# Kernel optimization log

Hardware: AMD Instinct MI355X
Metric: run time of the kernel (lower is better)

## Reference

```python
import jax, jax.numpy as jnp
import numpy as np

M = 256       # number of chart centers
D = 512       # feature dim
B = 131072    # batch of encoder features
R = 32.0      # chart radius (~sqrt(2*D) for whitened random data)
TAU = 0.01    # center EMA rate
EPS = 1e-6


def setup_inputs() -> dict:
    key = jax.random.key(0)
    k0, k1, k2, k3 = jax.random.split(key, 4)
    z = jax.random.normal(k0, (B, D), dtype=jnp.float32)
    centers = jax.random.normal(k1, (M, D), dtype=jnp.float32)
    stats_mean = 0.1 * jax.random.normal(k2, (D,), dtype=jnp.float32)
    stats_var = jax.random.uniform(k3, (D,), dtype=jnp.float32, minval=0.5, maxval=1.5)
    return {"z": z, "centers": centers, "stats_mean": stats_mean, "stats_var": stats_var}


def _whiten(z, mean, var):
    return (z - mean) / jnp.sqrt(var + EPS)


def _cdist(z_w, centers):
    # ||a-c||^2 = ||a||^2 + ||c||^2 - 2 a.c   (avoids [B,M,D] intermediate)
    zn = jnp.sum(z_w * z_w, axis=1)            # [B]
    cn = jnp.sum(centers * centers, axis=1)     # [M]
    d2 = zn[:, None] + cn[None, :] - 2.0 * (z_w @ centers.T)  # [B, M]
    return jnp.sqrt(jnp.maximum(d2, 0.0))


def reference(z, centers, stats_mean, stats_var):
    # memberships(): whiten + cdist + argmin + radius masks
    z_w = _whiten(z, stats_mean, stats_var)     # [B, D]
    dists = _cdist(z_w, centers)                # [B, M]
    hard_idx = jnp.argmin(dists, axis=1)        # [B]
    masks = dists <= R                          # [B, M] bool (masks[:, i] == torch masks[i])

    # soft_update_centers(): scatter-mean of z_w per nearest cluster, EMA update
    counts = jax.ops.segment_sum(jnp.ones((z_w.shape[0],), z_w.dtype), hard_idx, num_segments=M)  # [M]
    sums = jax.ops.segment_sum(z_w, hard_idx, num_segments=M)                                     # [M, D]
    mean_i = sums / jnp.maximum(counts, 1.0)[:, None]
    has_members = (counts > 0)[:, None]
    new_centers = jnp.where(has_members, (1.0 - TAU) * centers + TAU * mean_i, centers)

    return dists, hard_idx, masks, new_centers
```

## Files before the change

kernel.cpp:

```cpp
#include <hip/hip_runtime.h>
#include <math.h>

#define M_CENTERS 256
#define D_DIM     512
#define B_BATCH   131072
#define RADIUS    32.0f
#define TAU_F     0.01f
#define EPS_F     1e-6f

#define DMARGIN 2.0e-2f
#define REF_BLOCKS 1024
#define UCHUNKS 16
#define NCHUNK 16
#define SC_ROWS 1024

typedef __attribute__((ext_vector_type(8))) short bf16x8;
typedef __attribute__((ext_vector_type(16))) float f32x16;

__device__ __forceinline__ unsigned short bf16h(float x) {
    unsigned int u = __float_as_uint(x);
    return (unsigned short)((u + 0x7fffu + ((u >> 16) & 1u)) >> 16);
}
__device__ __forceinline__ unsigned cvt_pk_bf16(float a, float b) {
    unsigned r;
    asm("v_cvt_pk_bf16_f32 %0, %1, %2" : "=v"(r) : "v"(a), "v"(b));
    return r;
}

__global__ void prep_ss_kernel(const float* __restrict__ mean, const float* __restrict__ var,
                               float* __restrict__ scale, float* __restrict__ shift) {
    int d = blockIdx.x * 256 + threadIdx.x;
    if (d < D_DIM) {
        float s = 1.0f / sqrtf(var[d] + EPS_F);
        scale[d] = s;
        shift[d] = -mean[d] * s;
    }
}

__global__ void prep_cb_kernel(const float* __restrict__ centers, unsigned char* __restrict__ img,
                               float* __restrict__ cn) {
    int c = blockIdx.x;
    int l = threadIdx.x;
    int kc = l >> 2, kq = l & 3;
    const float* cp = centers + (size_t)c * D_DIM + kc * 32 + kq * 8;
    float4 a = *reinterpret_cast<const float4*>(cp);
    float4 b = *reinterpret_cast<const float4*>(cp + 4);
    float s = a.x*a.x + a.y*a.y + a.z*a.z + a.w*a.w + b.x*b.x + b.y*b.y + b.z*b.z + b.w*b.w;
    #pragma unroll
    for (int off = 32; off >= 1; off >>= 1) s += __shfl_xor(s, off, 64);
    if (l == 0) cn[c] = s;

    unsigned h0 = cvt_pk_bf16(a.x, a.y);
    unsigned h1 = cvt_pk_bf16(a.z, a.w);
    unsigned h2 = cvt_pk_bf16(b.x, b.y);
    unsigned h3 = cvt_pk_bf16(b.z, b.w);
    *reinterpret_cast<uint4*>(img + (size_t)kc * 16384 + (size_t)kq * 4096 + (size_t)c * 16) =
        make_uint4(h0, h1, h2, h3);
}

__global__ __launch_bounds__(256, 4)
void dist_mfma_kernel(const float* __restrict__ z,
                      const unsigned char* __restrict__ cb_img,
                      const float* __restrict__ scale, const float* __restrict__ shift,
                      const float* __restrict__ cn,
                      float* __restrict__ out_dists, float* __restrict__ out_idxf,
                      float* __restrict__ out_masks, int* __restrict__ ws_idx,
                      int* __restrict__ counts,
                      int* __restrict__ amb_count, int* __restrict__ amb_rows) {
    __shared__ union {
        struct { unsigned char A[2][4096]; unsigned char B[2][16384]; } p;
        float bounce[2][16][256];
        struct { float znrow[64]; float rminS[64][2]; int ridxS[64][2];
                 int rcntS[64][2]; float fminS[64]; int lhist[M_CENTERS]; } e;
    } sm;

    const int tid = threadIdx.x;
    const int wv = tid >> 6, lane = tid & 63;
    const int rt = wv >> 1, ch = wv & 1;
    const int l31 = lane & 31, kg = lane >> 5;
    const int b0 = blockIdx.x * 64;

    const int arow = tid >> 2, akq = tid & 3;
    const float* zrow = z + (size_t)(b0 + arow) * D_DIM;

    f32x16 acc[4];
    #pragma unroll
    for (int n = 0; n < 4; ++n)
        #pragma unroll
        for (int r = 0; r < 16; ++r) acc[n][r] = 0.0f;
    float zsq = 0.0f;
    float4 zv, zv2, scv, scv2, shv, shv2;

    auto stage_load = [&](int kc, int cb) {
        const unsigned char* bsrc = cb_img + (size_t)kc * 16384 + (size_t)wv * 4096;
        unsigned char* bdst = &sm.p.B[cb][wv * 4096];
        #pragma unroll
        for (int r = 0; r < 4; ++r) {
            __builtin_amdgcn_global_load_lds(
                (const __attribute__((address_space(1))) unsigned int*)(bsrc + r * 1024 + (lane << 4)),
                (__attribute__((address_space(3))) unsigned int*)(bdst + r * 1024),
                16, 0, 0);
        }
        const int kf = kc * 32 + akq * 8;
        zv   = *reinterpret_cast<const float4*>(zrow + kf);
        zv2  = *reinterpret_cast<const float4*>(zrow + kf + 4);
        scv  = *reinterpret_cast<const float4*>(scale + kf);
        scv2 = *reinterpret_cast<const float4*>(scale + kf + 4);
        shv  = *reinterpret_cast<const float4*>(shift + kf);
        shv2 = *reinterpret_cast<const float4*>(shift + kf + 4);
    };
    auto stage_write = [&](int cb) {
        float w0 = fmaf(zv.x,  scv.x,  shv.x);
        float w1 = fmaf(zv.y,  scv.y,  shv.y);
        float w2 = fmaf(zv.z,  scv.z,  shv.z);
        float w3 = fmaf(zv.w,  scv.w,  shv.w);
        float w4 = fmaf(zv2.x, scv2.x, shv2.x);
        float w5 = fmaf(zv2.y, scv2.y, shv2.y);
        float w6 = fmaf(zv2.z, scv2.z, shv2.z);
        float w7 = fmaf(zv2.w, scv2.w, shv2.w);
        zsq = fmaf(w0, w0, fmaf(w1, w1, fmaf(w2, w2, fmaf(w3, w3, zsq))));
        zsq = fmaf(w4, w4, fmaf(w5, w5, fmaf(w6, w6, fmaf(w7, w7, zsq))));
        uint4 hv = make_uint4(cvt_pk_bf16(w0, w1), cvt_pk_bf16(w2, w3),
                              cvt_pk_bf16(w4, w5), cvt_pk_bf16(w6, w7));
        *reinterpret_cast<uint4*>(&sm.p.A[cb][akq * 1024 + arow * 16]) = hv;
    };

    stage_load(0, 0);
    stage_write(0);
    __syncthreads();

    int cc = 0;
    for (int kc = 0; kc < NCHUNK; ++kc) {
        const bool pf = (kc + 1 < NCHUNK);
        if (pf) stage_load(kc + 1, cc ^ 1);
        const unsigned char* Ab = &sm.p.A[cc][0];
        const unsigned char* Bb = &sm.p.B[cc][0];
        const int arow16 = (rt * 32 + l31) * 16;
        bf16x8 a0 = *reinterpret_cast<const bf16x8*>(Ab + (0 * 2 + kg) * 1024 + arow16);
        bf16x8 a1 = *reinterpret_cast<const bf16x8*>(Ab + (1 * 2 + kg) * 1024 + arow16);
        #pragma unroll
        for (int n = 0; n < 4; ++n) {
            const int bcol16 = (ch * 128 + n * 32 + l31) * 16;
            bf16x8 b0 = *reinterpret_cast<const bf16x8*>(Bb + (0 * 2 + kg) * 4096 + bcol16);
            bf16x8 b1 = *reinterpret_cast<const bf16x8*>(Bb + (1 * 2 + kg) * 4096 + bcol16);
            acc[n] = __builtin_amdgcn_mfma_f32_32x32x16_bf16(a0, b0, acc[n], 0, 0, 0);
            acc[n] = __builtin_amdgcn_mfma_f32_32x32x16_bf16(a1, b1, acc[n], 0, 0, 0);
        }
        if (pf) stage_write(cc ^ 1);
        __syncthreads();
        cc ^= 1;
    }

    zsq += __shfl_xor(zsq, 1, 64);
    zsq += __shfl_xor(zsq, 2, 64);
    if (akq == 0) sm.e.znrow[arow] = zsq;
    sm.e.lhist[tid] = 0;
    __syncthreads();

    float znv[16];
    #pragma unroll
    for (int r = 0; r < 16; ++r) znv[r] = sm.e.znrow[rt * 32 + 4 * kg + (r & 3) + 8 * (r >> 2)];
    float cnv[4];
    #pragma unroll
    for (int n = 0; n < 4; ++n) cnv[n] = cn[ch * 128 + n * 32 + l31];

    #pragma unroll
    for (int n = 0; n < 4; ++n)
        #pragma unroll
        for (int r = 0; r < 16; ++r) {
            float d2 = znv[r] + cnv[n] - 2.0f * acc[n][r];
            acc[n][r] = sqrtf(fmaxf(d2, 0.0f));
        }

    #pragma unroll
    for (int r = 0; r < 16; ++r) {
        float bd = 3.4e38f; int bi = 0;
        #pragma unroll
        for (int n = 0; n < 4; ++n) {
            float d = acc[n][r];
            int col = ch * 128 + n * 32 + l31;
            if (d < bd) { bd = d; bi = col; }
        }
        #pragma unroll
        for (int off = 1; off <= 16; off <<= 1) {
            float od = __shfl_xor(bd, off, 64);
            int   oi = __shfl_xor(bi, off, 64);
            if (od < bd || (od == bd && oi < bi)) { bd = od; bi = oi; }
        }
        if (l31 == 0) {
            int R = rt * 32 + 4 * kg + (r & 3) + 8 * (r >> 2);
            sm.e.rminS[R][ch] = bd; sm.e.ridxS[R][ch] = bi;
        }
    }
    __syncthreads();
    if (tid < 64) {
        float d0 = sm.e.rminS[tid][0], d1 = sm.e.rminS[tid][1];
        int i0 = sm.e.ridxS[tid][0], i1 = sm.e.ridxS[tid][1];
        float fd = d0; int fi = i0;
        if (d1 < d0 || (d1 == d0 && i1 < i0)) { fd = d1; fi = i1; }
        sm.e.fminS[tid] = fd;
        out_idxf[b0 + tid] = (float)fi;
        ws_idx[b0 + tid] = fi;
        atomicAdd(&sm.e.lhist[fi], 1);
    }
    __syncthreads();
    #pragma unroll
    for (int r = 0; r < 16; ++r) {
        int R = rt * 32 + 4 * kg + (r & 3) + 8 * (r >> 2);
        float thr = sm.e.fminS[R] + DMARGIN;
        int cnt = 0;
        #pragma unroll
        for (int n = 0; n < 4; ++n) cnt += (acc[n][r] <= thr) ? 1 : 0;
        #pragma unroll
        for (int off = 1; off <= 16; off <<= 1) cnt += __shfl_xor(cnt, off, 64);
        if (l31 == 0) sm.e.rcntS[R][ch] = cnt;
    }
    __syncthreads();
    if (tid < 64) {
        if (sm.e.rcntS[tid][0] + sm.e.rcntS[tid][1] > 1) {
            int p = atomicAdd(amb_count, 1);
            if (p < B_BATCH) amb_rows[p] = b0 + tid;
        }
    }
    if (sm.e.lhist[tid] > 0) atomicAdd(&counts[tid], sm.e.lhist[tid]);

    #pragma unroll
    for (int hp = 0; hp < 2; ++hp) {
        __syncthreads();
        #pragma unroll
        for (int rr = 0; rr < 8; ++rr) {
            const int r = hp * 8 + rr;
            const int Rl = 4 * kg + (r & 3) + 8 * (r >> 2) - hp * 16;
            #pragma unroll
            for (int n = 0; n < 4; ++n)
                sm.bounce[rt][Rl][ch * 128 + n * 32 + l31] = acc[n][r];
        }
        __syncthreads();
        #pragma unroll
        for (int i = 0; i < 8; ++i) {
            const int Rl = ch * 8 + i;
            float4 dq = *reinterpret_cast<const float4*>(&sm.bounce[rt][Rl][lane * 4]);
            const int grow = b0 + rt * 32 + hp * 16 + Rl;
            size_t ob = (size_t)grow * M_CENTERS + lane * 4;
            *reinterpret_cast<float4*>(out_dists + ob) = dq;
            float4 mq = make_float4(dq.x <= RADIUS ? 1.0f : 0.0f, dq.y <= RADIUS ? 1.0f : 0.0f,
                                    dq.z <= RADIUS ? 1.0f : 0.0f, dq.w <= RADIUS ? 1.0f : 0.0f);
            *reinterpret_cast<float4*>(out_masks + ob) = mq;
        }
    }
}

__global__ __launch_bounds__(64)
void refine_kernel(const float* __restrict__ z, const float* __restrict__ centers,
                   const float* __restrict__ smean, const float* __restrict__ svar,
                   const float* __restrict__ dists,
                   const int* __restrict__ amb_count, const int* __restrict__ amb_rows,
                   float* __restrict__ out_idxf, int* __restrict__ ws_idx,
                   int* __restrict__ counts) {
    const int lane = threadIdx.x;
    int n = *amb_count;
    if (n > B_BATCH) n = B_BATCH;
    for (int e = blockIdx.x; e < n; e += REF_BLOCKS) {
        const int row = amb_rows[e];
        float4 dq = *reinterpret_cast<const float4*>(dists + (size_t)row * M_CENTERS + lane * 4);
        float dl[4] = { dq.x, dq.y, dq.z, dq.w };
        float dmin = fminf(fminf(dl[0], dl[1]), fminf(dl[2], dl[3]));
        #pragma unroll
        for (int off = 32; off >= 1; off >>= 1) dmin = fminf(dmin, __shfl_xor(dmin, off, 64));

        float zwf[8];
        double zn = 0.0;
        {
            float4 za = *reinterpret_cast<const float4*>(z + (size_t)row * D_DIM + lane * 8);
            float4 zb = *reinterpret_cast<const float4*>(z + (size_t)row * D_DIM + lane * 8 + 4);
            float zr[8] = { za.x, za.y, za.z, za.w, zb.x, zb.y, zb.z, zb.w };
            #pragma unroll
            for (int k = 0; k < 8; ++k) {
                int d = lane * 8 + k;
                float w = (zr[k] - smean[d]) / sqrtf(svar[d] + EPS_F);
                zwf[k] = w;
                zn += (double)w * (double)w;
            }
        }
        #pragma unroll
        for (int off = 32; off >= 1; off >>= 1) zn += __shfl_xor(zn, off, 64);
        const float zn32 = (float)zn;

        float bestd = 3.4e38f;
        int bestj = M_CENTERS;
        #pragma unroll
        for (int q = 0; q < 4; ++q) {
            unsigned long long mask = __ballot(dl[q] <= dmin + DMARGIN);
            while (mask) {
                int b = __ffsll(mask) - 1;
                mask &= mask - 1;
                int j = b * 4 + q;
                float4 ca = *reinterpret_cast<const float4*>(centers + (size_t)j * D_DIM + lane * 8);
                float4 cb = *reinterpret_cast<const float4*>(centers + (size_t)j * D_DIM + lane * 8 + 4);
                float cr[8] = { ca.x, ca.y, ca.z, ca.w, cb.x, cb.y, cb.z, cb.w };
                double dot = 0.0, cnl = 0.0;
                #pragma unroll
                for (int k = 0; k < 8; ++k) {
                    double c = (double)cr[k];
                    dot += (double)zwf[k] * c;
                    cnl += c * c;
                }
                #pragma unroll
                for (int off = 32; off >= 1; off >>= 1) {
                    dot += __shfl_xor(dot, off, 64);
                    cnl += __shfl_xor(cnl, off, 64);
                }
                float cn32  = (float)cnl;
                float dot32 = (float)dot;
                float t1  = zn32 + cn32;
                float d2f = t1 - 2.0f * dot32;
                d2f = fmaxf(d2f, 0.0f);
                float df = sqrtf(d2f);
                if (df < bestd || (df == bestd && j < bestj)) { bestd = df; bestj = j; }
            }
        }
        if (lane == 0) {
            int old = ws_idx[row];
            if (old != bestj) {
                atomicSub(&counts[old], 1);
                atomicAdd(&counts[bestj], 1);
                out_idxf[row] = (float)bestj;
                ws_idx[row]   = bestj;
            }
        }
    }
}

__global__ void scan_kernel(const int* __restrict__ counts, int* __restrict__ offsets,
                            int* __restrict__ cursor) {
    __shared__ int s[M_CENTERS];
    int t = threadIdx.x;
    int c = counts[t];
    s[t] = c;
    __syncthreads();
    for (int off = 1; off < M_CENTERS; off <<= 1) {
        int v = (t >= off) ? s[t - off] : 0;
        __syncthreads();
        s[t] += v;
        __syncthreads();
    }
    int excl = s[t] - c;
    offsets[t] = excl;
    cursor[t]  = excl;
    if (t == M_CENTERS - 1) offsets[M_CENTERS] = s[t];
}

__global__ __launch_bounds__(256)
void scatter2_kernel(const int* __restrict__ idx, int* __restrict__ cursor,
                     int* __restrict__ order) {
    __shared__ int lh[M_CENTERS];
    __shared__ int lb[M_CENTERS];
    const int t = threadIdx.x;
    lh[t] = 0;
    __syncthreads();
    const int base = blockIdx.x * SC_ROWS;
    int m[4], pl[4];
    #pragma unroll
    for (int k = 0; k < 4; ++k) {
        m[k] = idx[base + k * 256 + t];
        pl[k] = atomicAdd(&lh[m[k]], 1);
    }
    __syncthreads();
    int c = lh[t];
    if (c > 0) lb[t] = atomicAdd(&cursor[t], c);
    __syncthreads();
    #pragma unroll
    for (int k = 0; k < 4; ++k)
        order[lb[m[k]] + pl[k]] = base + k * 256 + t;
}

__global__ __launch_bounds__(128)
void update_partial_kernel(const float* __restrict__ z,
                           const float* __restrict__ scale, const float* __restrict__ shift,
                           const int* __restrict__ offsets, const int* __restrict__ order,
                           float* __restrict__ partial) {
    const int m = blockIdx.x / UCHUNKS;
    const int c = blockIdx.x % UCHUNKS;
    const int t = threadIdx.x;
    const int d0 = t * 4;
    const int start = offsets[m], end = offsets[m + 1];
    const int len = end - start;
    const int cs = (len + UCHUNKS - 1) / UCHUNKS;
    const int s0 = start + c * cs;
    int s1 = s0 + cs; if (s1 > end) s1 = end;

    const float4 sc = *reinterpret_cast<const float4*>(scale + d0);
    const float4 sh = *reinterpret_cast<const float4*>(shift + d0);
    float a0 = 0.0f, a1 = 0.0f, a2 = 0.0f, a3 = 0.0f;
    int i = s0;
    for (; i + 4 <= s1; i += 4) {
        int b0 = order[i], b1 = order[i + 1], b2 = order[i + 2], b3 = order[i + 3];
        float4 v0 = *reinterpret_cast<const float4*>(z + (size_t)b0 * D_DIM + d0);
        float4 v1 = *reinterpret_cast<const float4*>(z + (size_t)b1 * D_DIM + d0);
        float4 v2 = *reinterpret_cast<const float4*>(z + (size_t)b2 * D_DIM + d0);
        float4 v3 = *reinterpret_cast<const float4*>(z + (size_t)b3 * D_DIM + d0);
        a0 += fmaf(v0.x, sc.x, sh.x); a1 += fmaf(v0.y, sc.y, sh.y);
        a2 += fmaf(v0.z, sc.z, sh.z); a3 += fmaf(v0.w, sc.w, sh.w);
        a0 += fmaf(v1.x, sc.x, sh.x); a1 += fmaf(v1.y, sc.y, sh.y);
        a2 += fmaf(v1.z, sc.z, sh.z); a3 += fmaf(v1.w, sc.w, sh.w);
        a0 += fmaf(v2.x, sc.x, sh.x); a1 += fmaf(v2.y, sc.y, sh.y);
        a2 += fmaf(v2.z, sc.z, sh.z); a3 += fmaf(v2.w, sc.w, sh.w);
        a0 += fmaf(v3.x, sc.x, sh.x); a1 += fmaf(v3.y, sc.y, sh.y);
        a2 += fmaf(v3.z, sc.z, sh.z); a3 += fmaf(v3.w, sc.w, sh.w);
    }
    for (; i < s1; ++i) {
        int b = order[i];
        float4 v = *reinterpret_cast<const float4*>(z + (size_t)b * D_DIM + d0);
        a0 += fmaf(v.x, sc.x, sh.x); a1 += fmaf(v.y, sc.y, sh.y);
        a2 += fmaf(v.z, sc.z, sh.z); a3 += fmaf(v.w, sc.w, sh.w);
    }
    *reinterpret_cast<float4*>(partial + ((size_t)blockIdx.x) * D_DIM + d0) =
        make_float4(a0, a1, a2, a3);
}

__global__ __launch_bounds__(128)
void update_reduce_kernel(const float* __restrict__ centers,
                          const int* __restrict__ offsets,
                          const float* __restrict__ partial,
                          float* __restrict__ out_nc) {
    const int m = blockIdx.x;
    const int t = threadIdx.x;
    const int d0 = t * 4;
    const int cnt = offsets[m + 1] - offsets[m];
    float a0 = 0.0f, a1 = 0.0f, a2 = 0.0f, a3 = 0.0f;
    #pragma unroll
    for (int c = 0; c < UCHUNKS; ++c) {
        float4 v = *reinterpret_cast<const float4*>(partial + ((size_t)(m * UCHUNKS + c)) * D_DIM + d0);
        a0 += v.x; a1 += v.y; a2 += v.z; a3 += v.w;
    }
    float4 cv = *reinterpret_cast<const float4*>(centers + (size_t)m * D_DIM + d0);
    float4 r = cv;
    if (cnt > 0) {
        float inv = 1.0f / (float)cnt;
        r.x = (1.0f - TAU_F) * cv.x + TAU_F * (a0 * inv);
        r.y = (1.0f - TAU_F) * cv.y + TAU_F * (a1 * inv);
        r.z = (1.0f - TAU_F) * cv.z + TAU_F * (a2 * inv);
        r.w = (1.0f - TAU_F) * cv.w + TAU_F * (a3 * inv);
    }
    *reinterpret_cast<float4*>(out_nc + (size_t)m * D_DIM + d0) = r;
}

extern "C" void kernel_launch(void* const* d_in, const int* in_sizes, int n_in,
                              void* d_out, int out_size, void* d_ws, size_t ws_size,
                              hipStream_t stream) {
    const float* z       = (const float*)d_in[0];
    const float* centers = (const float*)d_in[1];
    const float* smean   = (const float*)d_in[2];
    const float* svar    = (const float*)d_in[3];

    float* out = (float*)d_out;
    float* out_dists = out;
    float* out_idxf  = out + (size_t)B_BATCH * M_CENTERS;
    float* out_masks = out_idxf + B_BATCH;
    float* out_nc    = out_masks + (size_t)B_BATCH * M_CENTERS;

    char* wsp = (char*)d_ws;
    float* scale   = (float*)wsp; wsp += D_DIM * sizeof(float);
    float* shift   = (float*)wsp; wsp += D_DIM * sizeof(float);
    float* cn      = (float*)wsp; wsp += M_CENTERS * sizeof(float);
    int* ws_idx    = (int*)wsp;   wsp += (size_t)B_BATCH * sizeof(int);
    int* counts    = (int*)wsp;   wsp += M_CENTERS * sizeof(int);
    int* amb_count = (int*)wsp;   wsp += 4 * sizeof(int);
    int* offsets   = (int*)wsp;   wsp += (M_CENTERS + 4) * sizeof(int);
    int* cursor    = (int*)wsp;   wsp += M_CENTERS * sizeof(int);
    int* order     = (int*)wsp;   wsp += (size_t)B_BATCH * sizeof(int);
    int* amb_rows  = (int*)wsp;   wsp += (size_t)B_BATCH * sizeof(int);
    float* partial = (float*)wsp; wsp += (size_t)M_CENTERS * UCHUNKS * D_DIM * sizeof(float);
    unsigned char* cb_img = (unsigned char*)wsp; wsp += (size_t)NCHUNK * 16384;

    prep_ss_kernel<<<2, 256, 0, stream>>>(smean, svar, scale, shift);
    prep_cb_kernel<<<M_CENTERS, 64, 0, stream>>>(centers, cb_img, cn);
    hipMemsetAsync(counts, 0, (M_CENTERS + 4) * sizeof(int), stream);
    dist_mfma_kernel<<<B_BATCH / 64, 256, 0, stream>>>(z, cb_img, scale, shift, cn,
                                                       out_dists, out_idxf, out_masks, ws_idx,
                                                       counts, amb_count, amb_rows);
    refine_kernel<<<REF_BLOCKS, 64, 0, stream>>>(z, centers, smean, svar, out_dists,
                                                 amb_count, amb_rows, out_idxf, ws_idx, counts);
    scan_kernel<<<1, 256, 0, stream>>>(counts, offsets, cursor);
    scatter2_kernel<<<B_BATCH / SC_ROWS, 256, 0, stream>>>(ws_idx, cursor, order);
    update_partial_kernel<<<M_CENTERS * UCHUNKS, 128, 0, stream>>>(z, scale, shift,
                                                                   offsets, order, partial);
    update_reduce_kernel<<<M_CENTERS, 128, 0, stream>>>(centers, offsets, partial, out_nc);
}
```

Measured before the change: 308.7 us.

## Prefetch z two chunks ahead in dist kernel; replace sort-based center update with slab atomics

The distance kernel now loads z rows two K-chunks ahead into a double register buffer and uses a custom barrier that waits only for older vector loads (vmcnt(2)), so global latency overlaps the MFMA work. Separately, the scan, scatter and gather-by-order update path is replaced by one slab kernel. Each block owns a 32-wide feature slice and a row chunk and accumulates whitened values per center with LDS atomics, followed by a small EMA reduce over the row chunks. This removes two kernel launches and the indirect gathers. The cost is scalar non-coalesced 4-byte z loads and LDS atomic contention on popular centers.

Measured after the change: 853.3 us. +176.4%, slower.

```diff
diff --git a/kernel.cpp b/kernel.cpp
--- a/kernel.cpp
+++ b/kernel.cpp
@@ -10,17 +10,13 @@
 
 #define DMARGIN 2.0e-2f
 #define REF_BLOCKS 1024
-#define UCHUNKS 16
 #define NCHUNK 16
-#define SC_ROWS 1024
+#define DSL 16
+#define RCH 16
 
 typedef __attribute__((ext_vector_type(8))) short bf16x8;
 typedef __attribute__((ext_vector_type(16))) float f32x16;
 
-__device__ __forceinline__ unsigned short bf16h(float x) {
-    unsigned int u = __float_as_uint(x);
-    return (unsigned short)((u + 0x7fffu + ((u >> 16) & 1u)) >> 16);
-}
 __device__ __forceinline__ unsigned cvt_pk_bf16(float a, float b) {
     unsigned r;
     asm("v_cvt_pk_bf16_f32 %0, %1, %2" : "=v"(r) : "v"(a), "v"(b));
@@ -89,9 +85,11 @@
         #pragma unroll
         for (int r = 0; r < 16; ++r) acc[n][r] = 0.0f;
     float zsq = 0.0f;
-    float4 zv, zv2, scv, scv2, shv, shv2;
-
-    auto stage_load = [&](int kc, int cb) {
+
+    float4 zbuf[2][2];
+    float4 scv[2], shv[2];
+
+    auto issue_glds = [&](int kc, int cb) {
         const unsigned char* bsrc = cb_img + (size_t)kc * 16384 + (size_t)wv * 4096;
         unsigned char* bdst = &sm.p.B[cb][wv * 4096];
         #pragma unroll
@@ -101,40 +99,37 @@
                 (__attribute__((address_space(3))) unsigned int*)(bdst + r * 1024),
                 16, 0, 0);
         }
+    };
+    auto load_scsh = [&](int kc) {
         const int kf = kc * 32 + akq * 8;
-        zv   = *reinterpret_cast<const float4*>(zrow + kf);
-        zv2  = *reinterpret_cast<const float4*>(zrow + kf + 4);
-        scv  = *reinterpret_cast<const float4*>(scale + kf);
-        scv2 = *reinterpret_cast<const float4*>(scale + kf + 4);
-        shv  = *reinterpret_cast<const float4*>(shift + kf);
-        shv2 = *reinterpret_cast<const float4*>(shift + kf + 4);
-    };
-    auto stage_write = [&](int cb) {
-        float w0 = fmaf(zv.x,  scv.x,  shv.x);
-        float w1 = fmaf(zv.y,  scv.y,  shv.y);
-        float w2 = fmaf(zv.z,  scv.z,  shv.z);
-        float w3 = fmaf(zv.w,  scv.w,  shv.w);
-        float w4 = fmaf(zv2.x, scv2.x, shv2.x);
-        float w5 = fmaf(zv2.y, scv2.y, shv2.y);
-        float w6 = fmaf(zv2.z, scv2.z, shv2.z);
-        float w7 = fmaf(zv2.w, scv2.w, shv2.w);
+        scv[0] = *reinterpret_cast<const float4*>(scale + kf);
+        scv[1] = *reinterpret_cast<const float4*>(scale + kf + 4);
+        shv[0] = *reinterpret_cast<const float4*>(shift + kf);
+        shv[1] = *reinterpret_cast<const float4*>(shift + kf + 4);
+    };
+    auto load_z = [&](int kc, int set) {
+        const int kf = kc * 32 + akq * 8;
+        zbuf[set][0] = *reinterpret_cast<const float4*>(zrow + kf);
+        zbuf[set][1] = *reinterpret_cast<const float4*>(zrow + kf + 4);
+    };
+    auto stage_write = [&](int cb, int set) {
+        float w0 = fmaf(zbuf[set][0].x, scv[0].x, shv[0].x);
+        float w1 = fmaf(zbuf[set][0].y, scv[0].y, shv[0].y);
+        float w2 = fmaf(zbuf[set][0].z, scv[0].z, shv[0].z);
+        float w3 = fmaf(zbuf[set][0].w, scv[0].w, shv[0].w);
+        float w4 = fmaf(zbuf[set][1].x, scv[1].x, shv[1].x);
+        float w5 = fmaf(zbuf[set][1].y, scv[1].y, shv[1].y);
+        float w6 = fmaf(zbuf[set][1].z, scv[1].z, shv[1].z);
+        float w7 = fmaf(zbuf[set][1].w, scv[1].w, shv[1].w);
         zsq = fmaf(w0, w0, fmaf(w1, w1, fmaf(w2, w2, fmaf(w3, w3, zsq))));
         zsq = fmaf(w4, w4, fmaf(w5, w5, fmaf(w6, w6, fmaf(w7, w7, zsq))));
         uint4 hv = make_uint4(cvt_pk_bf16(w0, w1), cvt_pk_bf16(w2, w3),
                               cvt_pk_bf16(w4, w5), cvt_pk_bf16(w6, w7));
         *reinterpret_cast<uint4*>(&sm.p.A[cb][akq * 1024 + arow * 16]) = hv;
     };
-
-    stage_load(0, 0);
-    stage_write(0);
-    __syncthreads();
-
-    int cc = 0;
-    for (int kc = 0; kc < NCHUNK; ++kc) {
-        const bool pf = (kc + 1 < NCHUNK);
-        if (pf) stage_load(kc + 1, cc ^ 1);
-        const unsigned char* Ab = &sm.p.A[cc][0];
-        const unsigned char* Bb = &sm.p.B[cc][0];
+    auto mfma_block = [&](int cb) {
+        const unsigned char* Ab = &sm.p.A[cb][0];
+        const unsigned char* Bb = &sm.p.B[cb][0];
         const int arow16 = (rt * 32 + l31) * 16;
         bf16x8 a0 = *reinterpret_cast<const bf16x8*>(Ab + (0 * 2 + kg) * 1024 + arow16);
         bf16x8 a1 = *reinterpret_cast<const bf16x8*>(Ab + (1 * 2 + kg) * 1024 + arow16);
@@ -146,10 +141,32 @@
             acc[n] = __builtin_amdgcn_mfma_f32_32x32x16_bf16(a0, b0, acc[n], 0, 0, 0);
             acc[n] = __builtin_amdgcn_mfma_f32_32x32x16_bf16(a1, b1, acc[n], 0, 0, 0);
         }
-        if (pf) stage_write(cc ^ 1);
-        __syncthreads();
-        cc ^= 1;
-    }
+    };
+    auto pipe_barrier = [&]() {
+        asm volatile("s_waitcnt vmcnt(2) lgkmcnt(0)" ::: "memory");
+        __builtin_amdgcn_s_barrier();
+        asm volatile("" ::: "memory");
+        __builtin_amdgcn_sched_barrier(0);
+    };
+
+    issue_glds(0, 0);
+    load_scsh(0);
+    load_z(0, 0);
+    load_z(1, 1);
+    stage_write(0, 0);
+    pipe_barrier();
+
+    #pragma unroll
+    for (int kc = 0; kc < NCHUNK - 1; ++kc) {
+        const int cur = kc & 1, nxt = cur ^ 1;
+        issue_glds(kc + 1, nxt);
+        load_scsh(kc + 1);
+        load_z((kc + 2 < NCHUNK) ? kc + 2 : NCHUNK - 1, kc & 1);
+        mfma_block(cur);
+        stage_write(nxt, (kc + 1) & 1);
+        pipe_barrier();
+    }
+    mfma_block((NCHUNK - 1) & 1);
 
     zsq += __shfl_xor(zsq, 1, 64);
     zsq += __shfl_xor(zsq, 2, 64);
@@ -331,106 +348,55 @@
     }
 }
 
-__global__ void scan_kernel(const int* __restrict__ counts, int* __restrict__ offsets,
-                            int* __restrict__ cursor) {
-    __shared__ int s[M_CENTERS];
-    int t = threadIdx.x;
-    int c = counts[t];
-    s[t] = c;
-    __syncthreads();
-    for (int off = 1; off < M_CENTERS; off <<= 1) {
-        int v = (t >= off) ? s[t - off] : 0;
-        __syncthreads();
-        s[t] += v;
-        __syncthreads();
-    }
-    int excl = s[t] - c;
-    offsets[t] = excl;
-    cursor[t]  = excl;
-    if (t == M_CENTERS - 1) offsets[M_CENTERS] = s[t];
-}
-
 __global__ __launch_bounds__(256)
-void scatter2_kernel(const int* __restrict__ idx, int* __restrict__ cursor,
-                     int* __restrict__ order) {
-    __shared__ int lh[M_CENTERS];
-    __shared__ int lb[M_CENTERS];
-    const int t = threadIdx.x;
-    lh[t] = 0;
-    __syncthreads();
-    const int base = blockIdx.x * SC_ROWS;
-    int m[4], pl[4];
-    #pragma unroll
-    for (int k = 0; k < 4; ++k) {
-        m[k] = idx[base + k * 256 + t];
-        pl[k] = atomicAdd(&lh[m[k]], 1);
-    }
-    __syncthreads();
-    int c = lh[t];
-    if (c > 0) lb[t] = atomicAdd(&cursor[t], c);
-    __syncthreads();
-    #pragma unroll
-    for (int k = 0; k < 4; ++k)
-        order[lb[m[k]] + pl[k]] = base + k * 256 + t;
+void update_slab_kernel(const float* __restrict__ z,
+                        const float* __restrict__ scale, const float* __restrict__ shift,
+                        const int* __restrict__ ws_idx, float* __restrict__ partial) {
+    __shared__ float lsum[M_CENTERS][32];
+    const int ds = blockIdx.x & (DSL - 1);
+    const int rc = blockIdx.x >> 4;
+    const int tid = threadIdx.x;
+    const int lane_d = tid & 31, rgrp = tid >> 5;
+    const int d0 = ds * 32 + lane_d;
+
+    #pragma unroll
+    for (int m = rgrp; m < M_CENTERS; m += 8) lsum[m][lane_d] = 0.0f;
+    __syncthreads();
+
+    const float sc = scale[d0], sh = shift[d0];
+    const int rows = B_BATCH / RCH;
+    const int base = rc * rows;
+    for (int r = rgrp; r < rows; r += 32) {
+        int row0 = base + r, row1 = row0 + 8, row2 = row0 + 16, row3 = row0 + 24;
+        int m0 = ws_idx[row0], m1 = ws_idx[row1], m2 = ws_idx[row2], m3 = ws_idx[row3];
+        float v0 = z[(size_t)row0 * D_DIM + d0];
+        float v1 = z[(size_t)row1 * D_DIM + d0];
+        float v2 = z[(size_t)row2 * D_DIM + d0];
+        float v3 = z[(size_t)row3 * D_DIM + d0];
+        atomicAdd(&lsum[m0][lane_d], fmaf(v0, sc, sh));
+        atomicAdd(&lsum[m1][lane_d], fmaf(v1, sc, sh));
+        atomicAdd(&lsum[m2][lane_d], fmaf(v2, sc, sh));
+        atomicAdd(&lsum[m3][lane_d], fmaf(v3, sc, sh));
+    }
+    __syncthreads();
+    #pragma unroll
+    for (int m = rgrp; m < M_CENTERS; m += 8)
+        partial[((size_t)rc * M_CENTERS + m) * D_DIM + d0] = lsum[m][lane_d];
 }
 
 __global__ __launch_bounds__(128)
-void update_partial_kernel(const float* __restrict__ z,
-                           const float* __restrict__ scale, const float* __restrict__ shift,
-                           const int* __restrict__ offsets, const int* __restrict__ order,
-                           float* __restrict__ partial) {
-    const int m = blockIdx.x / UCHUNKS;
-    const int c = blockIdx.x % UCHUNKS;
-    const int t = threadIdx.x;
-    const int d0 = t * 4;
-    const int start = offsets[m], end = offsets[m + 1];
-    const int len = end - start;
-    const int cs = (len + UCHUNKS - 1) / UCHUNKS;
-    const int s0 = start + c * cs;
-    int s1 = s0 + cs; if (s1 > end) s1 = end;
-
-    const float4 sc = *reinterpret_cast<const float4*>(scale + d0);
-    const float4 sh = *reinterpret_cast<const float4*>(shift + d0);
-    float a0 = 0.0f, a1 = 0.0f, a2 = 0.0f, a3 = 0.0f;
-    int i = s0;
-    for (; i + 4 <= s1; i += 4) {
-        int b0 = order[i], b1 = order[i + 1], b2 = order[i + 2], b3 = order[i + 3];
-        float4 v0 = *reinterpret_cast<const float4*>(z + (size_t)b0 * D_DIM + d0);
-        float4 v1 = *reinterpret_cast<const float4*>(z + (size_t)b1 * D_DIM + d0);
-        float4 v2 = *reinterpret_cast<const float4*>(z + (size_t)b2 * D_DIM + d0);
-        float4 v3 = *reinterpret_cast<const float4*>(z + (size_t)b3 * D_DIM + d0);
-        a0 += fmaf(v0.x, sc.x, sh.x); a1 += fmaf(v0.y, sc.y, sh.y);
-        a2 += fmaf(v0.z, sc.z, sh.z); a3 += fmaf(v0.w, sc.w, sh.w);
-        a0 += fmaf(v1.x, sc.x, sh.x); a1 += fmaf(v1.y, sc.y, sh.y);
-        a2 += fmaf(v1.z, sc.z, sh.z); a3 += fmaf(v1.w, sc.w, sh.w);
-        a0 += fmaf(v2.x, sc.x, sh.x); a1 += fmaf(v2.y, sc.y, sh.y);
-        a2 += fmaf(v2.z, sc.z, sh.z); a3 += fmaf(v2.w, sc.w, sh.w);
-        a0 += fmaf(v3.x, sc.x, sh.x); a1 += fmaf(v3.y, sc.y, sh.y);
-        a2 += fmaf(v3.z, sc.z, sh.z); a3 += fmaf(v3.w, sc.w, sh.w);
-    }
-    for (; i < s1; ++i) {
-        int b = order[i];
-        float4 v = *reinterpret_cast<const float4*>(z + (size_t)b * D_DIM + d0);
-        a0 += fmaf(v.x, sc.x, sh.x); a1 += fmaf(v.y, sc.y, sh.y);
-        a2 += fmaf(v.z, sc.z, sh.z); a3 += fmaf(v.w, sc.w, sh.w);
-    }
-    *reinterpret_cast<float4*>(partial + ((size_t)blockIdx.x) * D_DIM + d0) =
-        make_float4(a0, a1, a2, a3);
-}
-
-__global__ __launch_bounds__(128)
-void update_reduce_kernel(const float* __restrict__ centers,
-                          const int* __restrict__ offsets,
-                          const float* __restrict__ partial,
-                          float* __restrict__ out_nc) {
+void ema_reduce_kernel(const float* __restrict__ centers,
+                       const int* __restrict__ counts,
+                       const float* __restrict__ partial,
+                       float* __restrict__ out_nc) {
     const int m = blockIdx.x;
     const int t = threadIdx.x;
     const int d0 = t * 4;
-    const int cnt = offsets[m + 1] - offsets[m];
+    const int cnt = counts[m];
     float a0 = 0.0f, a1 = 0.0f, a2 = 0.0f, a3 = 0.0f;
     #pragma unroll
-    for (int c = 0; c < UCHUNKS; ++c) {
-        float4 v = *reinterpret_cast<const float4*>(partial + ((size_t)(m * UCHUNKS + c)) * D_DIM + d0);
+    for (int rc = 0; rc < RCH; ++rc) {
+        float4 v = *reinterpret_cast<const float4*>(partial + ((size_t)rc * M_CENTERS + m) * D_DIM + d0);
         a0 += v.x; a1 += v.y; a2 += v.z; a3 += v.w;
     }
     float4 cv = *reinterpret_cast<const float4*>(centers + (size_t)m * D_DIM + d0);
@@ -466,11 +432,8 @@
     int* ws_idx    = (int*)wsp;   wsp += (size_t)B_BATCH * sizeof(int);
     int* counts    = (int*)wsp;   wsp += M_CENTERS * sizeof(int);
     int* amb_count = (int*)wsp;   wsp += 4 * sizeof(int);
-    int* offsets   = (int*)wsp;   wsp += (M_CENTERS + 4) * sizeof(int);
-    int* cursor    = (int*)wsp;   wsp += M_CENTERS * sizeof(int);
-    int* order     = (int*)wsp;   wsp += (size_t)B_BATCH * sizeof(int);
     int* amb_rows  = (int*)wsp;   wsp += (size_t)B_BATCH * sizeof(int);
-    float* partial = (float*)wsp; wsp += (size_t)M_CENTERS * UCHUNKS * D_DIM * sizeof(float);
+    float* partial = (float*)wsp; wsp += (size_t)RCH * M_CENTERS * D_DIM * sizeof(float);
     unsigned char* cb_img = (unsigned char*)wsp; wsp += (size_t)NCHUNK * 16384;
 
     prep_ss_kernel<<<2, 256, 0, stream>>>(smean, svar, scale, shift);
@@ -481,9 +444,6 @@
                                                        counts, amb_count, amb_rows);
     refine_kernel<<<REF_BLOCKS, 64, 0, stream>>>(z, centers, smean, svar, out_dists,
                                                  amb_count, amb_rows, out_idxf, ws_idx, counts);
-    scan_kernel<<<1, 256, 0, stream>>>(counts, offsets, cursor);
-    scatter2_kernel<<<B_BATCH / SC_ROWS, 256, 0, stream>>>(ws_idx, cursor, order);
-    update_partial_kernel<<<M_CENTERS * UCHUNKS, 128, 0, stream>>>(z, scale, shift,
-                                                                   offsets, order, partial);
-    update_reduce_kernel<<<M_CENTERS, 128, 0, stream>>>(centers, offsets, partial, out_nc);
-}
+    update_slab_kernel<<<RCH * DSL, 256, 0, stream>>>(z, scale, shift, ws_idx, partial);
+    ema_reduce_kernel<<<M_CENTERS, 128, 0, stream>>>(centers, counts, partial, out_nc);
+}
```
